# Kernel tuning notes

Hardware: AMD Instinct MI355X
Metric: run time of the kernel (lower is better)

Reference implementation:

```python
import jax, jax.numpy as jnp
import numpy as np

BINS = 32
WIN = 9
SIGMA_RATIO = 1.0
_SIGMA = (1.0 / (BINS - 1)) * SIGMA_RATIO          # mean(diff(linspace(0,1,bins)))
PRETERM = 2.0 / (2.0 * _SIGMA ** 2)                # = 961 for bins=32, ratio=1
BIN_CENTERS = jnp.linspace(0.0, 1.0, BINS)


def _correlation_ratio(X, Y, win=WIN):
    B, C, H, W, D = Y.shape
    h_r, w_r, d_r = (-H) % win, (-W) % win, (-D) % win
    pad = ((0, 0), (0, 0),
           (h_r // 2, h_r - h_r // 2),
           (w_r // 2, w_r - w_r // 2),
           (d_r // 2, d_r - d_r // 2))
    X = jnp.pad(X, pad)
    Y = jnp.pad(Y, pad)
    B, C, H, W, D = Y.shape
    nH, nW, nD = H // win, W // win, D // win
    num_patch = nH * nW * nD

    def to_flat(T):
        T = T.reshape(B, C, nH, win, nW, win, nD, win)
        return T.transpose(0, 2, 4, 6, 1, 3, 5, 7).reshape(B * num_patch, C, win ** 3)

    x_flat = to_flat(X)                              # [P, C, w3]
    y_flat = to_flat(Y)                              # [P, C, w3]

    bins = BIN_CENTERS.astype(Y.dtype)
    diff = y_flat[:, :, None, :] - bins[None, None, :, None]   # [P, C, bins, w3]
    weights = jnp.exp(-PRETERM * jnp.square(diff))              # Parzen Gaussian
    weights_norm = weights / (jnp.sum(weights, axis=-1, keepdims=True) + 1e-5)

    mean_intensities = jnp.sum(weights_norm * x_flat[:, :, None, :], axis=3)  # [P, C, bins]
    bin_counts = jnp.sum(weights, axis=3)                                     # [P, C, bins]
    total_mean = jnp.mean(x_flat, axis=2, keepdims=True)                      # [P, C, 1]

    between_group_variance = (
        jnp.sum(bin_counts * (mean_intensities - total_mean) ** 2, axis=2)
        / jnp.sum(bin_counts, axis=2)
    )                                                                          # [P, C]
    total_variance = jnp.var(x_flat, axis=2, ddof=1)                           # unbiased, like torch.var
    eta_square = between_group_variance / (total_variance + 1e-5)
    return jnp.mean(eta_square) / 3.0


def reference(y_true, y_pred):
    CR = _correlation_ratio(y_true, y_pred) + _correlation_ratio(y_pred, y_true)
    s = WIN // 2
    yt = jnp.roll(y_true, shift=(-s, -s, -s), axis=(2, 3, 4))
    yp = jnp.roll(y_pred, shift=(-s, -s, -s), axis=(2, 3, 4))
    CR_shifted = _correlation_ratio(yt, yp) + _correlation_ratio(yp, yt)
    return -CR / 4.0 - CR_shifted / 4.0


def setup_inputs() -> dict:
    key = jax.random.key(0)
    k1, k2 = jax.random.split(key)
    shape = (1, 1, 90, 90, 90)
    y_true = jax.random.uniform(k1, shape, dtype=jnp.float32)
    y_pred = jax.random.uniform(k2, shape, dtype=jnp.float32)
    return {"y_true": y_true, "y_pred": y_pred}
```

## Files before the change

### kernel.cpp

```cpp
#include <hip/hip_runtime.h>


constexpr int   NPATCH = 1000;
constexpr int   WIN3   = 729;
constexpr float PRETERM = 961.0f;

__global__ __launch_bounds__(256)
void cr_patch_kernel(const float* __restrict__ yt,
                     const float* __restrict__ yp,
                     float* __restrict__ etas)
{
    __shared__ float sx[WIN3];
    __shared__ float sy[WIN3];
    __shared__ float red[8];
    __shared__ float swA [4][32];
    __shared__ float swxA[4][32];

    const int bid  = blockIdx.x;
    const int conf = bid / NPATCH;
    const int p    = bid - conf * NPATCH;
    const int ph   = p / 100;
    const int pw   = (p / 10) % 10;
    const int pd   = p % 10;

    const float* X = (conf & 1) ? yp : yt;
    const float* Y = (conf & 1) ? yt : yp;
    const int shift = (conf >= 2) ? 4 : 0;

    const int tid  = threadIdx.x;
    const int wid  = tid >> 6;
    const int lane = tid & 63;

    float sumx = 0.f, sumx2 = 0.f;
    for (int j = tid; j < WIN3; j += 256) {
        int dh  = j / 81;
        int rem = j - dh * 81;
        int dw  = rem / 9;
        int dd  = rem - dw * 9;
        int H = ph * 9 + dh + shift; if (H >= 90) H -= 90;
        int W = pw * 9 + dw + shift; if (W >= 90) W -= 90;
        int D = pd * 9 + dd + shift; if (D >= 90) D -= 90;
        int idx = (H * 90 + W) * 90 + D;
        float xv = X[idx];
        float yv = Y[idx];
        sx[j] = xv;
        sy[j] = yv;
        sumx  += xv;
        sumx2  = fmaf(xv, xv, sumx2);
    }
    #pragma unroll
    for (int m = 1; m < 64; m <<= 1) {
        sumx  += __shfl_xor(sumx,  m);
        sumx2 += __shfl_xor(sumx2, m);
    }
    if (lane == 0) { red[wid * 2] = sumx; red[wid * 2 + 1] = sumx2; }
    __syncthreads();

    const float tot_x  = red[0] + red[2] + red[4] + red[6];
    const float tot_x2 = red[1] + red[3] + red[5] + red[7];
    const float mean   = tot_x * (1.0f / 729.0f);

    const int   bin = lane & 31;
    const int   grp = wid * 2 + (lane >> 5);
    const float c   = (float)bin * (1.0f / 31.0f);

    float sw = 0.f, swx = 0.f;
    for (int j = grp; j < WIN3; j += 8) {
        float yv = sy[j];
        float xv = sx[j];
        float d  = yv - c;
        float w  = __expf(-PRETERM * d * d);
        sw += w;
        swx = fmaf(w, xv, swx);
    }
    sw  += __shfl_xor(sw,  32);
    swx += __shfl_xor(swx, 32);
    if (lane < 32) { swA[wid][bin] = sw; swxA[wid][bin] = swx; }
    __syncthreads();

    if (tid < 32) {
        float Sw  = swA [0][tid] + swA [1][tid] + swA [2][tid] + swA [3][tid];
        float Swx = swxA[0][tid] + swxA[1][tid] + swxA[2][tid] + swxA[3][tid];
        float mi  = Swx / (Sw + 1e-5f);
        float dmu = mi - mean;
        float t   = Sw * dmu * dmu;
        float ts  = Sw;
        #pragma unroll
        for (int m = 1; m < 32; m <<= 1) {
            t  += __shfl_xor(t,  m);
            ts += __shfl_xor(ts, m);
        }
        if (tid == 0) {
            float bgv = t / ts;
            float tv  = (tot_x2 - tot_x * tot_x * (1.0f / 729.0f)) * (1.0f / 728.0f);
            etas[bid] = bgv / (tv + 1e-5f);
        }
    }
}

__global__ __launch_bounds__(256)
void cr_reduce_kernel(const float* __restrict__ etas, float* __restrict__ out)
{
    __shared__ float red[4];
    float s = 0.f;
    for (int i = threadIdx.x; i < 4 * NPATCH; i += 256) s += etas[i];
    #pragma unroll
    for (int m = 1; m < 64; m <<= 1) s += __shfl_xor(s, m);
    if ((threadIdx.x & 63) == 0) red[threadIdx.x >> 6] = s;
    __syncthreads();
    if (threadIdx.x == 0)
        out[0] = -(red[0] + red[1] + red[2] + red[3]) * (1.0f / 12000.0f);
}

extern "C" void kernel_launch(void* const* d_in, const int* in_sizes, int n_in,
                              void* d_out, int out_size, void* d_ws, size_t ws_size,
                              hipStream_t stream)
{
    const float* y_true = (const float*)d_in[0];
    const float* y_pred = (const float*)d_in[1];
    float* out  = (float*)d_out;
    float* etas = (float*)d_ws;

    cr_patch_kernel<<<4 * NPATCH, 256, 0, stream>>>(y_true, y_pred, etas);
    cr_reduce_kernel<<<1, 256, 0, stream>>>(etas, out);
}
```

Baseline: 89.80 us.

## Process each patch with one wavefront using register-resident voxels and shuffle rotation

Each patch is now handled by a single 64-lane wavefront. Each lane keeps its 12 voxels in registers, so shared memory and block-level syncthreads are no longer needed. The per-bin accumulation is restructured: each lane loops over all 32 bins in a rotated order and passes partial sums through a shuffle-based rotation, then the two half-waves are combined. This removes LDS traffic and barriers, but each lane now evaluates 32x12 exponentials and there are fewer threads per block. Padded lanes use y=10 so their weights underflow to zero.

```diff
diff --git a/kernel.cpp b/kernel.cpp
--- a/kernel.cpp
+++ b/kernel.cpp
@@ -1,21 +1,14 @@
 #include <hip/hip_runtime.h>
 
 
-constexpr int   NPATCH = 1000;
-constexpr int   WIN3   = 729;
+constexpr int   NPATCH  = 1000;
 constexpr float PRETERM = 961.0f;
 
-__global__ __launch_bounds__(256)
+__global__ __launch_bounds__(64)
 void cr_patch_kernel(const float* __restrict__ yt,
                      const float* __restrict__ yp,
                      float* __restrict__ etas)
 {
-    __shared__ float sx[WIN3];
-    __shared__ float sy[WIN3];
-    __shared__ float red[8];
-    __shared__ float swA [4][32];
-    __shared__ float swxA[4][32];
-
     const int bid  = blockIdx.x;
     const int conf = bid / NPATCH;
     const int p    = bid - conf * NPATCH;
@@ -23,16 +16,16 @@
     const int pw   = (p / 10) % 10;
     const int pd   = p % 10;
 
-    const float* X = (conf & 1) ? yp : yt;
-    const float* Y = (conf & 1) ? yt : yp;
+    const float* __restrict__ X = (conf & 1) ? yp : yt;
+    const float* __restrict__ Y = (conf & 1) ? yt : yp;
     const int shift = (conf >= 2) ? 4 : 0;
 
-    const int tid  = threadIdx.x;
-    const int wid  = tid >> 6;
-    const int lane = tid & 63;
+    const int lane = threadIdx.x;
 
+    float xs[12], ys[12];
     float sumx = 0.f, sumx2 = 0.f;
-    for (int j = tid; j < WIN3; j += 256) {
+
+    auto load_voxel = [&](int j, float& xv, float& yv) {
         int dh  = j / 81;
         int rem = j - dh * 81;
         int dw  = rem / 9;
@@ -41,60 +34,67 @@
         int W = pw * 9 + dw + shift; if (W >= 90) W -= 90;
         int D = pd * 9 + dd + shift; if (D >= 90) D -= 90;
         int idx = (H * 90 + W) * 90 + D;
-        float xv = X[idx];
-        float yv = Y[idx];
-        sx[j] = xv;
-        sy[j] = yv;
-        sumx  += xv;
-        sumx2  = fmaf(xv, xv, sumx2);
+        xv = X[idx];
+        yv = Y[idx];
+    };
+
+    #pragma unroll
+    for (int v = 0; v < 11; ++v) {
+        load_voxel(lane + (v << 6), xs[v], ys[v]);
+        sumx  += xs[v];
+        sumx2  = fmaf(xs[v], xs[v], sumx2);
     }
+    if (lane < 729 - 11 * 64) {
+        load_voxel(lane + 704, xs[11], ys[11]);
+        sumx  += xs[11];
+        sumx2  = fmaf(xs[11], xs[11], sumx2);
+    } else {
+        xs[11] = 0.f;
+        ys[11] = 10.f;
+    }
+
     #pragma unroll
     for (int m = 1; m < 64; m <<= 1) {
         sumx  += __shfl_xor(sumx,  m);
         sumx2 += __shfl_xor(sumx2, m);
     }
-    if (lane == 0) { red[wid * 2] = sumx; red[wid * 2 + 1] = sumx2; }
-    __syncthreads();
+    const float mean = sumx * (1.0f / 729.0f);
 
-    const float tot_x  = red[0] + red[2] + red[4] + red[6];
-    const float tot_x2 = red[1] + red[3] + red[5] + red[7];
-    const float mean   = tot_x * (1.0f / 729.0f);
+    const int l5 = lane & 31;
+    const int hi = lane & 32;
+    float r_sw = 0.f, r_swx = 0.f;
 
-    const int   bin = lane & 31;
-    const int   grp = wid * 2 + (lane >> 5);
-    const float c   = (float)bin * (1.0f / 31.0f);
+    for (int k = 0; k < 32; ++k) {
+        const int   b = (l5 + k) & 31;
+        const float c = (float)b * (1.0f / 31.0f);
+        float sw = 0.f, swx = 0.f;
+        #pragma unroll
+        for (int v = 0; v < 12; ++v) {
+            float d = ys[v] - c;
+            float w = __expf(-PRETERM * d * d);
+            sw += w;
+            swx = fmaf(w, xs[v], swx);
+        }
+        const int src = hi | ((l5 - k) & 31);
+        r_sw  += __shfl(sw,  src, 64);
+        r_swx += __shfl(swx, src, 64);
+    }
+    r_sw  += __shfl_xor(r_sw,  32);
+    r_swx += __shfl_xor(r_swx, 32);
 
-    float sw = 0.f, swx = 0.f;
-    for (int j = grp; j < WIN3; j += 8) {
-        float yv = sy[j];
-        float xv = sx[j];
-        float d  = yv - c;
-        float w  = __expf(-PRETERM * d * d);
-        sw += w;
-        swx = fmaf(w, xv, swx);
+    float mi  = r_swx / (r_sw + 1e-5f);
+    float dmu = mi - mean;
+    float tn  = r_sw * dmu * dmu;
+    float td  = r_sw;
+    #pragma unroll
+    for (int m = 1; m < 32; m <<= 1) {
+        tn += __shfl_xor(tn, m);
+        td += __shfl_xor(td, m);
     }
-    sw  += __shfl_xor(sw,  32);
-    swx += __shfl_xor(swx, 32);
-    if (lane < 32) { swA[wid][bin] = sw; swxA[wid][bin] = swx; }
-    __syncthreads();
-
-    if (tid < 32) {
-        float Sw  = swA [0][tid] + swA [1][tid] + swA [2][tid] + swA [3][tid];
-        float Swx = swxA[0][tid] + swxA[1][tid] + swxA[2][tid] + swxA[3][tid];
-        float mi  = Swx / (Sw + 1e-5f);
-        float dmu = mi - mean;
-        float t   = Sw * dmu * dmu;
-        float ts  = Sw;
-        #pragma unroll
-        for (int m = 1; m < 32; m <<= 1) {
-            t  += __shfl_xor(t,  m);
-            ts += __shfl_xor(ts, m);
-        }
-        if (tid == 0) {
-            float bgv = t / ts;
-            float tv  = (tot_x2 - tot_x * tot_x * (1.0f / 729.0f)) * (1.0f / 728.0f);
-            etas[bid] = bgv / (tv + 1e-5f);
-        }
+    if (lane == 0) {
+        float bgv = tn / td;
+        float tv  = (sumx2 - sumx * sumx * (1.0f / 729.0f)) * (1.0f / 728.0f);
+        etas[bid] = bgv / (tv + 1e-5f);
     }
 }
 
@@ -121,6 +121,6 @@
     float* out  = (float*)d_out;
     float* etas = (float*)d_ws;
 
-    cr_patch_kernel<<<4 * NPATCH, 256, 0, stream>>>(y_true, y_pred, etas);
+    cr_patch_kernel<<<4 * NPATCH, 64, 0, stream>>>(y_true, y_pred, etas);
     cr_reduce_kernel<<<1, 256, 0, stream>>>(etas, out);
 }
```

New measurement: 89.52 us. About the same (-0.3%).
